# Performance work log

Hardware: AMD Instinct MI355X
Metric: run time of the kernel (lower is better)

## Reference

```python
import jax, jax.numpy as jnp
import numpy as np

COMMITMENT_COST = 0.25


def setup_inputs() -> dict:
    key = jax.random.key(0)
    k1, k2 = jax.random.split(key)
    inputs = jax.random.normal(k1, (32, 64, 32, 32), dtype=jnp.float32)  # (B, C, H, W)
    embed = jax.random.normal(k2, (64, 1024), dtype=jnp.float32)          # (embedding_dim, num_embeddings)
    return {"inputs": inputs, "embed": embed}


def reference(inputs, embed):
    # Eval-mode forward (EMA buffer updates are training-only side effects).
    B, C, H, W = inputs.shape
    K = embed.shape[1]
    flat = inputs.transpose(0, 2, 3, 1).reshape(-1, C)  # (N, C)
    N = flat.shape[0]

    distances = (jnp.sum(flat * flat, axis=1, keepdims=True)
                 + jnp.sum(embed * embed, axis=0)
                 - 2.0 * flat @ embed)
    encoding_indices = jnp.argmin(distances, axis=1)  # (N,)

    # Gather instead of one-hot @ embed.T (same math, no N x K one-hot)
    quantized = embed.T[encoding_indices]  # (N, C)

    e_latent_loss = jnp.mean((jax.lax.stop_gradient(quantized) - flat) ** 2)
    loss = COMMITMENT_COST * e_latent_loss

    # straight-through estimator
    quantized_st = flat + jax.lax.stop_gradient(quantized - flat)
    quantized_out = quantized_st.reshape(B, H, W, C).transpose(0, 3, 1, 2)

    # avg_probs via scatter-add counts (== mean of one-hot encodings)
    counts = jnp.zeros((K,), dtype=flat.dtype).at[encoding_indices].add(1.0)
    avg_probs = counts / N
    perplexity = jnp.exp(-jnp.sum(avg_probs * jnp.log(avg_probs + 1e-10)))

    return quantized_out, loss, encoding_indices, perplexity
```

## Files before the change

kernel.cpp:

```cpp
#include <hip/hip_runtime.h>

#define N_PIX  32768
#define C_DIM  64
#define K_EMB  1024
#define HW     1024
#define PIXB   64

#define OUT_Q_OFF    0
#define OUT_LOSS_OFF 2097152
#define OUT_IDX_OFF  2097153
#define OUT_PERP_OFF 2129921

typedef __attribute__((ext_vector_type(8)))  __bf16 bf16x8;
typedef __attribute__((ext_vector_type(16))) float  f32x16;

__device__ unsigned short g_esplit[3 * K_EMB * C_DIM];
__device__ uint4          g_eesplit[2 * K_EMB];
__device__ float          g_ee[K_EMB];
__device__ unsigned int   g_counts[K_EMB];
__device__ float          g_lossAcc;

__device__ __forceinline__ unsigned short f2bf(float f) {
    unsigned u = __float_as_uint(f);
    unsigned r = u + 0x7FFFu + ((u >> 16) & 1u);
    return (unsigned short)(r >> 16);
}
__device__ __forceinline__ float bf2f(unsigned short b) {
    return __uint_as_float(((unsigned)b) << 16);
}
__device__ __forceinline__ unsigned long long pack_score(float d, int k) {
    unsigned int u = __float_as_uint(d);
    u = (u & 0x80000000u) ? ~u : (u | 0x80000000u);
    return ((unsigned long long)u << 32) | (unsigned int)k;
}
__device__ __forceinline__ uint4 pack8(const unsigned short* v) {
    uint4 u;
    u.x = (unsigned)v[0] | ((unsigned)v[1] << 16);
    u.y = (unsigned)v[2] | ((unsigned)v[3] << 16);
    u.z = (unsigned)v[4] | ((unsigned)v[5] << 16);
    u.w = (unsigned)v[6] | ((unsigned)v[7] << 16);
    return u;
}
__device__ __forceinline__ unsigned long long shfl_xor32_u64(unsigned long long v) {
    unsigned lo = (unsigned)v, hi = (unsigned)(v >> 32);
    lo = __shfl_xor(lo, 32, 64);
    hi = __shfl_xor(hi, 32, 64);
    return ((unsigned long long)hi << 32) | lo;
}
#define UPD2(P1, P2, MM) { \
    if ((MM) < P1) { P2 = P1; P1 = (MM); } else if ((MM) < P2) P2 = (MM); }
#define MRG2(P1, P2, O1, O2) { \
    unsigned long long _lo = (O1) < P1 ? (O1) : P1; \
    unsigned long long _hi = (O1) < P1 ? P1 : (O1); \
    unsigned long long _m2 = (O2) < P2 ? (O2) : P2; \
    P1 = _lo; P2 = _hi < _m2 ? _hi : _m2; }

__global__ void k_prep(const float* __restrict__ embed) {
    const int code = blockIdx.x * 64 + threadIdx.x;
    if (code == 0) g_lossAcc = 0.f;
    g_counts[code] = 0u;
    const int tile = code >> 5, c32 = code & 31;
    uint4* o = reinterpret_cast<uint4*>(g_esplit);
    float ee = 0.f;
#pragma unroll
    for (int s = 0; s < 4; ++s)
#pragma unroll
        for (int hh = 0; hh < 2; ++hh) {
            unsigned short b1[8], b2[8], b3[8];
#pragma unroll
            for (int e = 0; e < 8; ++e) {
                const float x = embed[(s * 16 + hh * 8 + e) * K_EMB + code];
                ee = fmaf(x, x, ee);
                b1[e] = f2bf(x);
                const float r1 = x - bf2f(b1[e]);
                b2[e] = f2bf(r1);
                const float r2 = r1 - bf2f(b2[e]);
                b3[e] = f2bf(r2);
            }
            const int oi = tile * 256 + s * 64 + hh * 32 + c32;
            o[oi        ] = pack8(b1);
            o[oi +  8192] = pack8(b2);
            o[oi + 16384] = pack8(b3);
        }
    g_ee[code] = ee;
    const float v = -0.5f * ee;
    const unsigned short e1 = f2bf(v);
    const float r1 = v - bf2f(e1);
    const unsigned short e2 = f2bf(r1);
    const float r2 = r1 - bf2f(e2);
    const unsigned short e3 = f2bf(r2);
    g_eesplit[code] = make_uint4((unsigned)e1 | ((unsigned)e2 << 16),
                                 (unsigned)e3, 0u, 0u);
    g_eesplit[K_EMB + code] = make_uint4(0u, 0u, 0u, 0u);
}

__global__ __launch_bounds__(256, 2) void k_main(
    const float* __restrict__ inp, const float* __restrict__ embed,
    float* __restrict__ out_q, float* __restrict__ out_idx) {

    __shared__ float x_raw[C_DIM * PIXB];
    __shared__ uint4 xfrag[3 * 4 * 2 * PIXB];
    __shared__ unsigned long long red1[4][PIXB];
    __shared__ unsigned long long red2[4][PIXB];
    __shared__ int   ksel[PIXB];
    __shared__ float lred[4];
    __shared__ float bdist;

    const int tid = threadIdx.x;
    const int n0  = blockIdx.x * PIXB;
    const int b   = n0 >> 10;
    const int hw0 = n0 & 1023;
    const float* __restrict__ xg = inp + b * (C_DIM * HW) + hw0;

    const int w   = tid >> 6;
    const int ln  = tid & 63;
    const int c31 = ln & 31;
    const int h   = ln >> 5;
    const uint4* __restrict__ eg = reinterpret_cast<const uint4*>(g_esplit);
    const int abase = h * 32 + c31;

    uint4 pA[8], pAe, pB[8], pBe;
    {
        const int b0 = w * 256 + abase;
#pragma unroll
        for (int s = 0; s < 4; ++s) { pA[s] = eg[b0 + s * 64]; pA[4 + s] = eg[b0 + 8192 + s * 64]; }
        pAe = g_eesplit[h * K_EMB + w * 32 + c31];
    }

#pragma unroll
    for (int i = 0; i < 4; ++i) {
        const int F = tid + i * 256;
        const int c = F >> 4, p4 = (F & 15) << 2;
        *reinterpret_cast<float4*>(&x_raw[F << 2]) =
            *reinterpret_cast<const float4*>(xg + c * HW + p4);
    }
    __syncthreads();

    float sx2 = 0.f;
#pragma unroll
    for (int cc = 0; cc < 2; ++cc) {
        const int cid = tid + cc * 256;
        const int s = cid >> 7, hh = (cid >> 6) & 1, p = cid & 63;
        unsigned short b1[8], b2[8], b3[8];
#pragma unroll
        for (int e = 0; e < 8; ++e) {
            const float x = x_raw[(s * 16 + hh * 8 + e) * PIXB + p];
            sx2 = fmaf(x, x, sx2);
            b1[e] = f2bf(x);
            const float r1 = x - bf2f(b1[e]);
            b2[e] = f2bf(r1);
            const float r2 = r1 - bf2f(b2[e]);
            b3[e] = f2bf(r2);
        }
        const int fi = (s * 2 + hh) * PIXB + p;
        xfrag[fi            ] = pack8(b1);
        xfrag[fi + 8 * PIXB ] = pack8(b2);
        xfrag[fi + 16 * PIXB] = pack8(b3);
    }
    for (int off = 32; off; off >>= 1) sx2 += __shfl_down(sx2, off, 64);
    if ((tid & 63) == 0) lred[tid >> 6] = sx2;
    __syncthreads();

    unsigned long long p1a = ~0ull, p2a = ~0ull;
    unsigned long long p1b = ~0ull, p2b = ~0ull;
    const uint4 bones = make_uint4(h ? 0u : 0x3F803F80u, h ? 0u : 0x00003F80u, 0u, 0u);

#define MFMA1(AF, BF) \
    acc = __builtin_amdgcn_mfma_f32_32x32x16_bf16( \
        __builtin_bit_cast(bf16x8, AF), __builtin_bit_cast(bf16x8, BF), acc, 0, 0, 0);

#define STEP(CUR, CURE, NXT, NXTE, R) { \
    const int ct = (R) * 4 + w; \
    const int b0 = ct * 256 + abase; \
    uint4 a2[4]; \
    _Pragma("unroll") for (int s = 0; s < 4; ++s) a2[s] = eg[b0 + 16384 + s * 64]; \
    { const int rn = (R) < 7 ? (R) + 1 : 7; \
      const int bn = (rn * 4 + w) * 256 + abase; \
      _Pragma("unroll") for (int s = 0; s < 4; ++s) { \
          NXT[s] = eg[bn + s * 64]; NXT[4 + s] = eg[bn + 8192 + s * 64]; } \
      NXTE = g_eesplit[h * K_EMB + (rn * 4 + w) * 32 + c31]; } \
    const int cb = ct * 32; \
    _Pragma("unroll") for (int pt = 0; pt < 2; ++pt) { \
        const int pbase = pt * 32 + c31; \
        f32x16 acc = {}; \
        MFMA1(CURE, bones) \
        uint4 bx0[4], bx1[4], bx2[4]; \
        _Pragma("unroll") for (int s = 0; s < 4; ++s) bx0[s] = xfrag[(     s * 2 + h) * PIXB + pbase]; \
        _Pragma("unroll") for (int s = 0; s < 4; ++s) { MFMA1(CUR[s], bx0[s]) }       \
        _Pragma("unroll") for (int s = 0; s < 4; ++s) { MFMA1(CUR[4 + s], bx0[s]) }   \
        _Pragma("unroll") for (int s = 0; s < 4; ++s) bx1[s] = xfrag[( 8 + s * 2 + h) * PIXB + pbase]; \
        _Pragma("unroll") for (int s = 0; s < 4; ++s) { MFMA1(CUR[s], bx1[s]) }       \
        _Pragma("unroll") for (int s = 0; s < 4; ++s) { MFMA1(CUR[4 + s], bx1[s]) }   \
        _Pragma("unroll") for (int s = 0; s < 4; ++s) bx2[s] = xfrag[(16 + s * 2 + h) * PIXB + pbase]; \
        _Pragma("unroll") for (int s = 0; s < 4; ++s) { MFMA1(CUR[s], bx2[s]) }       \
        _Pragma("unroll") for (int s = 0; s < 4; ++s) { MFMA1(a2[s], bx0[s]) }        \
        _Pragma("unroll") for (int rg = 0; rg < 16; ++rg) { \
            const unsigned long long mm = \
                pack_score(-acc[rg], cb + (rg & 3) + 8 * (rg >> 2) + 4 * h); \
            if (pt == 0) { UPD2(p1a, p2a, mm) } else { UPD2(p1b, p2b, mm) } \
        } \
    } }

#pragma unroll 1
    for (int rr = 0; rr < 4; ++rr) {
        STEP(pA, pAe, pB, pBe, 2 * rr)
        STEP(pB, pBe, pA, pAe, 2 * rr + 1)
    }
#undef STEP
#undef MFMA1

    {
        unsigned long long o1 = shfl_xor32_u64(p1a), o2 = shfl_xor32_u64(p2a);
        MRG2(p1a, p2a, o1, o2)
        o1 = shfl_xor32_u64(p1b); o2 = shfl_xor32_u64(p2b);
        MRG2(p1b, p2b, o1, o2)
        if (ln < 32) {
            red1[w][ln] = p1a; red2[w][ln] = p2a;
            red1[w][ln + 32] = p1b; red2[w][ln + 32] = p2b;
        }
    }
    __syncthreads();

    if (tid < PIXB) {
        unsigned long long M1 = red1[0][tid], M2 = red2[0][tid];
        MRG2(M1, M2, red1[1][tid], red2[1][tid])
        MRG2(M1, M2, red1[2][tid], red2[2][tid])
        MRG2(M1, M2, red1[3][tid], red2[3][tid])
        const int k1 = (int)(unsigned int)(M1 & 0xFFFFFFFFull);
        const int k2 = (int)(unsigned int)(M2 & 0xFFFFFFFFull);
        float d1 = 0.f, d2 = 0.f;
        const float* xcol = x_raw + tid;
#pragma unroll 8
        for (int c = 0; c < C_DIM; ++c) {
            const float xv = xcol[c * PIXB];
            d1 = fmaf(xv, embed[c * K_EMB + k1], d1);
            d2 = fmaf(xv, embed[c * K_EMB + k2], d2);
        }
        const float dist1 = fmaf(-2.f, d1, g_ee[k1]);
        const float dist2 = fmaf(-2.f, d2, g_ee[k2]);
        const unsigned long long s1 = pack_score(dist1, k1);
        const unsigned long long s2 = pack_score(dist2, k2);
        const int  k     = (s1 < s2) ? k1 : k2;
        const float distw = (s1 < s2) ? dist1 : dist2;
        ksel[tid] = k;
        out_idx[n0 + tid] = (float)k;
        atomicAdd(g_counts + k, 1u);
        float dist = distw;
        for (int off = 32; off; off >>= 1) dist += __shfl_down(dist, off, 64);
        if (tid == 0) bdist = dist;
    }
    __syncthreads();

    {
        const int c  = tid >> 2;
        const int p0 = (tid & 3) * 16;
        float* oq = out_q + b * (C_DIM * HW) + c * HW + hw0 + p0;
        const float* er = embed + c * K_EMB;
#pragma unroll
        for (int i = 0; i < 4; ++i) {
            float4 q;
            q.x = er[ksel[p0 + i * 4 + 0]];
            q.y = er[ksel[p0 + i * 4 + 1]];
            q.z = er[ksel[p0 + i * 4 + 2]];
            q.w = er[ksel[p0 + i * 4 + 3]];
            *reinterpret_cast<float4*>(oq + i * 4) = q;
        }
    }
    if (tid == 0)
        atomicAdd(&g_lossAcc, lred[0] + lred[1] + lred[2] + lred[3] + bdist);
}

__global__ __launch_bounds__(1024) void k_scalar(float* __restrict__ out_loss,
                                                 float* __restrict__ out_perp) {
    __shared__ float red[16];
    const int tid = threadIdx.x;
    float p = (float)g_counts[tid] * (1.0f / (float)N_PIX);
    float t = p * logf(p + 1e-10f);
    for (int off = 32; off; off >>= 1) t += __shfl_down(t, off, 64);
    if ((tid & 63) == 0) red[tid >> 6] = t;
    __syncthreads();
    if (tid == 0) {
        float s = 0.f;
#pragma unroll
        for (int i = 0; i < 16; ++i) s += red[i];
        *out_perp = expf(-s);
        *out_loss = 0.25f * g_lossAcc * (1.0f / (float)(N_PIX * C_DIM));
    }
}

extern "C" void kernel_launch(void* const* d_in, const int* in_sizes, int n_in,
                              void* d_out, int out_size, void* d_ws, size_t ws_size,
                              hipStream_t stream) {
    const float* inp   = (const float*)d_in[0];
    const float* embed = (const float*)d_in[1];
    float* out = (float*)d_out;

    k_prep<<<dim3(16), dim3(64), 0, stream>>>(embed);
    k_main<<<dim3(N_PIX / PIXB), dim3(256), 0, stream>>>(
        inp, embed, out + OUT_Q_OFF, out + OUT_IDX_OFF);
    k_scalar<<<dim3(1), dim3(1024), 0, stream>>>(out + OUT_LOSS_OFF,
                                                 out + OUT_PERP_OFF);
}
```

Measured before the change: 136.5 us.

## Use 8 waves per block and drop codebook register double-buffering

```diff
diff --git a/kernel.cpp b/kernel.cpp
--- a/kernel.cpp
+++ b/kernel.cpp
@@ -5,6 +5,7 @@
 #define K_EMB  1024
 #define HW     1024
 #define PIXB   64
+#define WAVES  8
 
 #define OUT_Q_OFF    0
 #define OUT_LOSS_OFF 2097152
@@ -94,16 +95,16 @@
     g_eesplit[K_EMB + code] = make_uint4(0u, 0u, 0u, 0u);
 }
 
-__global__ __launch_bounds__(256, 2) void k_main(
+__global__ __launch_bounds__(512, 4) void k_main(
     const float* __restrict__ inp, const float* __restrict__ embed,
     float* __restrict__ out_q, float* __restrict__ out_idx) {
 
     __shared__ float x_raw[C_DIM * PIXB];
     __shared__ uint4 xfrag[3 * 4 * 2 * PIXB];
-    __shared__ unsigned long long red1[4][PIXB];
-    __shared__ unsigned long long red2[4][PIXB];
+    __shared__ unsigned long long red1[WAVES][PIXB];
+    __shared__ unsigned long long red2[WAVES][PIXB];
     __shared__ int   ksel[PIXB];
-    __shared__ float lred[4];
+    __shared__ float lred[WAVES];
     __shared__ float bdist;
 
     const int tid = threadIdx.x;
@@ -112,24 +113,9 @@
     const int hw0 = n0 & 1023;
     const float* __restrict__ xg = inp + b * (C_DIM * HW) + hw0;
 
-    const int w   = tid >> 6;
-    const int ln  = tid & 63;
-    const int c31 = ln & 31;
-    const int h   = ln >> 5;
-    const uint4* __restrict__ eg = reinterpret_cast<const uint4*>(g_esplit);
-    const int abase = h * 32 + c31;
-
-    uint4 pA[8], pAe, pB[8], pBe;
-    {
-        const int b0 = w * 256 + abase;
-#pragma unroll
-        for (int s = 0; s < 4; ++s) { pA[s] = eg[b0 + s * 64]; pA[4 + s] = eg[b0 + 8192 + s * 64]; }
-        pAe = g_eesplit[h * K_EMB + w * 32 + c31];
-    }
-
-#pragma unroll
-    for (int i = 0; i < 4; ++i) {
-        const int F = tid + i * 256;
+#pragma unroll
+    for (int i = 0; i < 2; ++i) {
+        const int F = tid + i * 512;
         const int c = F >> 4, p4 = (F & 15) << 2;
         *reinterpret_cast<float4*>(&x_raw[F << 2]) =
             *reinterpret_cast<const float4*>(xg + c * HW + p4);
@@ -137,10 +123,8 @@
     __syncthreads();
 
     float sx2 = 0.f;
-#pragma unroll
-    for (int cc = 0; cc < 2; ++cc) {
-        const int cid = tid + cc * 256;
-        const int s = cid >> 7, hh = (cid >> 6) & 1, p = cid & 63;
+    {
+        const int s = tid >> 7, hh = (tid >> 6) & 1, p = tid & 63;
         unsigned short b1[8], b2[8], b3[8];
 #pragma unroll
         for (int e = 0; e < 8; ++e) {
@@ -161,6 +145,13 @@
     if ((tid & 63) == 0) lred[tid >> 6] = sx2;
     __syncthreads();
 
+    const int w   = tid >> 6;
+    const int ln  = tid & 63;
+    const int c31 = ln & 31;
+    const int h   = ln >> 5;
+    const uint4* __restrict__ eg = reinterpret_cast<const uint4*>(g_esplit);
+    const int abase = h * 32 + c31;
+
     unsigned long long p1a = ~0ull, p2a = ~0ull;
     unsigned long long p1b = ~0ull, p2b = ~0ull;
     const uint4 bones = make_uint4(h ? 0u : 0x3F803F80u, h ? 0u : 0x00003F80u, 0u, 0u);
@@ -169,44 +160,65 @@
     acc = __builtin_amdgcn_mfma_f32_32x32x16_bf16( \
         __builtin_bit_cast(bf16x8, AF), __builtin_bit_cast(bf16x8, BF), acc, 0, 0, 0);
 
-#define STEP(CUR, CURE, NXT, NXTE, R) { \
-    const int ct = (R) * 4 + w; \
-    const int b0 = ct * 256 + abase; \
-    uint4 a2[4]; \
-    _Pragma("unroll") for (int s = 0; s < 4; ++s) a2[s] = eg[b0 + 16384 + s * 64]; \
-    { const int rn = (R) < 7 ? (R) + 1 : 7; \
-      const int bn = (rn * 4 + w) * 256 + abase; \
-      _Pragma("unroll") for (int s = 0; s < 4; ++s) { \
-          NXT[s] = eg[bn + s * 64]; NXT[4 + s] = eg[bn + 8192 + s * 64]; } \
-      NXTE = g_eesplit[h * K_EMB + (rn * 4 + w) * 32 + c31]; } \
-    const int cb = ct * 32; \
-    _Pragma("unroll") for (int pt = 0; pt < 2; ++pt) { \
-        const int pbase = pt * 32 + c31; \
-        f32x16 acc = {}; \
-        MFMA1(CURE, bones) \
-        uint4 bx0[4], bx1[4], bx2[4]; \
-        _Pragma("unroll") for (int s = 0; s < 4; ++s) bx0[s] = xfrag[(     s * 2 + h) * PIXB + pbase]; \
-        _Pragma("unroll") for (int s = 0; s < 4; ++s) { MFMA1(CUR[s], bx0[s]) }       \
-        _Pragma("unroll") for (int s = 0; s < 4; ++s) { MFMA1(CUR[4 + s], bx0[s]) }   \
-        _Pragma("unroll") for (int s = 0; s < 4; ++s) bx1[s] = xfrag[( 8 + s * 2 + h) * PIXB + pbase]; \
-        _Pragma("unroll") for (int s = 0; s < 4; ++s) { MFMA1(CUR[s], bx1[s]) }       \
-        _Pragma("unroll") for (int s = 0; s < 4; ++s) { MFMA1(CUR[4 + s], bx1[s]) }   \
-        _Pragma("unroll") for (int s = 0; s < 4; ++s) bx2[s] = xfrag[(16 + s * 2 + h) * PIXB + pbase]; \
-        _Pragma("unroll") for (int s = 0; s < 4; ++s) { MFMA1(CUR[s], bx2[s]) }       \
-        _Pragma("unroll") for (int s = 0; s < 4; ++s) { MFMA1(a2[s], bx0[s]) }        \
-        _Pragma("unroll") for (int rg = 0; rg < 16; ++rg) { \
-            const unsigned long long mm = \
-                pack_score(-acc[rg], cb + (rg & 3) + 8 * (rg >> 2) + 4 * h); \
-            if (pt == 0) { UPD2(p1a, p2a, mm) } else { UPD2(p1b, p2b, mm) } \
-        } \
-    } }
-
 #pragma unroll 1
-    for (int rr = 0; rr < 4; ++rr) {
-        STEP(pA, pAe, pB, pBe, 2 * rr)
-        STEP(pB, pBe, pA, pAe, 2 * rr + 1)
-    }
-#undef STEP
+    for (int r = 0; r < 4; ++r) {
+        const int ct = r * 8 + w;
+        const int b0 = ct * 256 + abase;
+        const int cb = ct * 32;
+        uint4 ae0[4], ae1[4], a2[4], aee;
+#pragma unroll
+        for (int s = 0; s < 4; ++s) {
+            ae0[s] = eg[b0 + s * 64];
+            ae1[s] = eg[b0 + 8192 + s * 64];
+            a2[s]  = eg[b0 + 16384 + s * 64];
+        }
+        aee = g_eesplit[h * K_EMB + ct * 32 + c31];
+
+#pragma unroll
+        for (int pt = 0; pt < 2; ++pt) {
+            const int pbase = pt * 32 + c31;
+            f32x16 acc = {};
+            MFMA1(aee, bones)
+            {
+                uint4 bx[4];
+#pragma unroll
+                for (int s = 0; s < 4; ++s) bx[s] = xfrag[(s * 2 + h) * PIXB + pbase];
+#pragma unroll
+                for (int s = 0; s < 4; ++s) { MFMA1(ae0[s], bx[s]) }
+#pragma unroll
+                for (int s = 0; s < 4; ++s) { MFMA1(ae1[s], bx[s]) }
+            }
+            {
+                uint4 bx[4];
+#pragma unroll
+                for (int s = 0; s < 4; ++s) bx[s] = xfrag[(8 + s * 2 + h) * PIXB + pbase];
+#pragma unroll
+                for (int s = 0; s < 4; ++s) { MFMA1(ae0[s], bx[s]) }
+#pragma unroll
+                for (int s = 0; s < 4; ++s) { MFMA1(ae1[s], bx[s]) }
+            }
+            {
+                uint4 bx[4];
+#pragma unroll
+                for (int s = 0; s < 4; ++s) bx[s] = xfrag[(16 + s * 2 + h) * PIXB + pbase];
+#pragma unroll
+                for (int s = 0; s < 4; ++s) { MFMA1(ae0[s], bx[s]) }
+            }
+            {
+                uint4 bx[4];
+#pragma unroll
+                for (int s = 0; s < 4; ++s) bx[s] = xfrag[(s * 2 + h) * PIXB + pbase];
+#pragma unroll
+                for (int s = 0; s < 4; ++s) { MFMA1(a2[s], bx[s]) }
+            }
+#pragma unroll
+            for (int rg = 0; rg < 16; ++rg) {
+                const unsigned long long mm =
+                    pack_score(-acc[rg], cb + (rg & 3) + 8 * (rg >> 2) + 4 * h);
+                if (pt == 0) { UPD2(p1a, p2a, mm) } else { UPD2(p1b, p2b, mm) }
+            }
+        }
+    }
 #undef MFMA1
 
     {
@@ -223,9 +235,8 @@
 
     if (tid < PIXB) {
         unsigned long long M1 = red1[0][tid], M2 = red2[0][tid];
-        MRG2(M1, M2, red1[1][tid], red2[1][tid])
-        MRG2(M1, M2, red1[2][tid], red2[2][tid])
-        MRG2(M1, M2, red1[3][tid], red2[3][tid])
+#pragma unroll
+        for (int wv = 1; wv < WAVES; ++wv) { MRG2(M1, M2, red1[wv][tid], red2[wv][tid]) }
         const int k1 = (int)(unsigned int)(M1 & 0xFFFFFFFFull);
         const int k2 = (int)(unsigned int)(M2 & 0xFFFFFFFFull);
         float d1 = 0.f, d2 = 0.f;
@@ -240,7 +251,7 @@
         const float dist2 = fmaf(-2.f, d2, g_ee[k2]);
         const unsigned long long s1 = pack_score(dist1, k1);
         const unsigned long long s2 = pack_score(dist2, k2);
-        const int  k     = (s1 < s2) ? k1 : k2;
+        const int   k     = (s1 < s2) ? k1 : k2;
         const float distw = (s1 < s2) ? dist1 : dist2;
         ksel[tid] = k;
         out_idx[n0 + tid] = (float)k;
@@ -251,23 +262,25 @@
     }
     __syncthreads();
 
-    {
-        const int c  = tid >> 2;
-        const int p0 = (tid & 3) * 16;
+#pragma unroll
+    for (int i = 0; i < 2; ++i) {
+        const int F = tid + i * 512;
+        const int c = F >> 4, p0 = (F & 15) << 2;
         float* oq = out_q + b * (C_DIM * HW) + c * HW + hw0 + p0;
         const float* er = embed + c * K_EMB;
-#pragma unroll
-        for (int i = 0; i < 4; ++i) {
-            float4 q;
-            q.x = er[ksel[p0 + i * 4 + 0]];
-            q.y = er[ksel[p0 + i * 4 + 1]];
-            q.z = er[ksel[p0 + i * 4 + 2]];
-            q.w = er[ksel[p0 + i * 4 + 3]];
-            *reinterpret_cast<float4*>(oq + i * 4) = q;
-        }
-    }
-    if (tid == 0)
-        atomicAdd(&g_lossAcc, lred[0] + lred[1] + lred[2] + lred[3] + bdist);
+        float4 q;
+        q.x = er[ksel[p0 + 0]];
+        q.y = er[ksel[p0 + 1]];
+        q.z = er[ksel[p0 + 2]];
+        q.w = er[ksel[p0 + 3]];
+        *reinterpret_cast<float4*>(oq) = q;
+    }
+    if (tid == 0) {
+        float ls = bdist;
+#pragma unroll
+        for (int wv = 0; wv < WAVES; ++wv) ls += lred[wv];
+        atomicAdd(&g_lossAcc, ls);
+    }
 }
 
 __global__ __launch_bounds__(1024) void k_scalar(float* __restrict__ out_loss,
@@ -296,7 +309,7 @@
     float* out = (float*)d_out;
 
     k_prep<<<dim3(16), dim3(64), 0, stream>>>(embed);
-    k_main<<<dim3(N_PIX / PIXB), dim3(256), 0, stream>>>(
+    k_main<<<dim3(N_PIX / PIXB), dim3(512), 0, stream>>>(
         inp, embed, out + OUT_Q_OFF, out + OUT_IDX_OFF);
     k_scalar<<<dim3(1), dim3(1024), 0, stream>>>(out + OUT_LOSS_OFF,
                                                  out + OUT_PERP_OFF);
```

Result: slower. 187.9 us (+37.6%).
